# Kernel tuning notes

Measured on AMD Instinct MI355X. Metric: run time of the kernel, lower is better.

The kernel has to match this reference:

```python
import jax, jax.numpy as jnp
import numpy as np

NSLICES = 4
HID = 512
IN_FEAT = 342   # input_shape - 1 (last column is phase)
OUT = 311
BATCH = 256


def cubic(y0, y1, y2, y3, mu):
    # Catmull-Rom cubic interpolation, as in the original PFNN code
    return (
        (-0.5 * y0 + 1.5 * y1 - 1.5 * y2 + 0.5 * y3) * mu * mu * mu
        + (y0 - 2.5 * y1 + 2.0 * y2 - 0.5 * y3) * mu * mu
        + (-0.5 * y0 + 0.5 * y2) * mu
        + y1
    )


def setup_inputs() -> dict:
    key = jax.random.key(0)
    ks = jax.random.split(key, 7)
    x = jax.random.uniform(ks[0], (BATCH, IN_FEAT + 1), dtype=jnp.float32)
    s = 0.02
    W0 = jax.random.normal(ks[1], (NSLICES, HID, IN_FEAT), dtype=jnp.float32) * s
    b0 = jax.random.normal(ks[2], (NSLICES, HID), dtype=jnp.float32) * s
    W1 = jax.random.normal(ks[3], (NSLICES, HID, HID), dtype=jnp.float32) * s
    b1 = jax.random.normal(ks[4], (NSLICES, HID), dtype=jnp.float32) * s
    W2 = jax.random.normal(ks[5], (NSLICES, OUT, HID), dtype=jnp.float32) * s
    b2 = jax.random.normal(ks[6], (NSLICES, OUT), dtype=jnp.float32) * s
    return {"x": x, "W0": W0, "b0": b0, "W1": W1, "b1": b1, "W2": W2, "b2": b2}


def reference(x, W0, b0, W1, b1, W2, b2):
    phase = x[:, -1]                       # [B]
    pscale = NSLICES * phase
    mu = jnp.mod(pscale, 1.0)              # [B]
    i1 = jnp.floor(pscale).astype(jnp.int32) % NSLICES
    i0 = (i1 - 1) % NSLICES
    i2 = (i1 + 1) % NSLICES
    i3 = (i1 + 2) % NSLICES
    muW = mu[:, None, None]                # broadcast over (out, in)
    mub = mu[:, None]

    Wb0 = cubic(W0[i0], W0[i1], W0[i2], W0[i3], muW)   # [B, 512, 342]
    bb0 = cubic(b0[i0], b0[i1], b0[i2], b0[i3], mub)   # [B, 512]
    Wb1 = cubic(W1[i0], W1[i1], W1[i2], W1[i3], muW)   # [B, 512, 512]
    bb1 = cubic(b1[i0], b1[i1], b1[i2], b1[i3], mub)
    Wb2 = cubic(W2[i0], W2[i1], W2[i2], W2[i3], muW)   # [B, 311, 512]
    bb2 = cubic(b2[i0], b2[i1], b2[i2], b2[i3], mub)

    h = x[:, :-1]                                       # [B, 342]
    h = jax.nn.elu(jnp.einsum('boi,bi->bo', Wb0, h) + bb0)
    h = jax.nn.elu(jnp.einsum('boi,bi->bo', Wb1, h) + bb1)
    out = jnp.einsum('boi,bi->bo', Wb2, h) + bb2        # [B, 311]
    return out
```

## Files before the change

kernel.cpp:

```cpp
#include <hip/hip_runtime.h>
#include <math.h>

#define HID 512
#define IN_FEAT 342
#define OUTD 311
#define BATCH 256
#define XROW (IN_FEAT + 1)
#define KP0 352

typedef unsigned short u16;
typedef short bf16x8 __attribute__((ext_vector_type(8)));
typedef float f32x4 __attribute__((ext_vector_type(4)));

__device__ __forceinline__ u16 f2bf_rne(float v) {
    unsigned int x = __float_as_uint(v);
    unsigned int r = (x + 0x7fffu + ((x >> 16) & 1u)) >> 16;
    return (u16)r;
}
__device__ __forceinline__ float bf2f(u16 u) {
    return __uint_as_float(((unsigned int)u) << 16);
}

__device__ __forceinline__ void cvt8(const float* v, bf16x8& hi, bf16x8& lo) {
#pragma unroll
    for (int j = 0; j < 8; j++) {
        unsigned int xu = __float_as_uint(v[j]);
        unsigned int rnd = xu + 0x7fffu + ((xu >> 16) & 1u);
        hi[j] = (short)(rnd >> 16);
        float lof = v[j] - __uint_as_float(rnd & 0xffff0000u);
        lo[j] = (short)(__float_as_uint(lof) >> 16);
    }
}

template<int KCH, int KLDS, int FINAL, int L0>
__global__ __launch_bounds__(256, 2) void layer_direct(
    const float* __restrict__ W,
    int Kw, int Mreal, int Mb,
    const float* __restrict__ x,
    const u16* __restrict__ Hhi, const u16* __restrict__ Hlo,
    const float* __restrict__ bias,
    u16* __restrict__ Ohi, u16* __restrict__ Olo, float* __restrict__ outp)
{
    union SharedU {
        u16 h[2][16 * KLDS];
        float acc[4][16][17];
    };
    __shared__ SharedU sm;

    const int tid = (int)threadIdx.x;
    const int b0 = (int)blockIdx.x * 16;
    const int o0 = (int)blockIdx.y * 16;

    if (L0) {
        for (int idx = tid; idx < 16 * KP0; idx += 256) {
            int r = idx / KP0, k = idx - r * KP0;
            float v = (k < IN_FEAT) ? x[(size_t)(b0 + r) * XROW + k] : 0.f;
            u16 h = f2bf_rne(v);
            sm.h[0][r * KLDS + k] = h;
            sm.h[1][r * KLDS + k] = f2bf_rne(v - bf2f(h));
        }
    } else {
        constexpr int CH = KCH * 4;
        for (int idx = tid; idx < 16 * CH; idx += 256) {
            int r = idx / CH, c = idx - r * CH;
            size_t g = (size_t)(b0 + r) * HID + c * 8;
            *reinterpret_cast<uint4*>(&sm.h[0][r * KLDS + c * 8]) =
                *reinterpret_cast<const uint4*>(Hhi + g);
            *reinterpret_cast<uint4*>(&sm.h[1][r * KLDS + c * 8]) =
                *reinterpret_cast<const uint4*>(Hlo + g);
        }
    }
    __syncthreads();

    const int lane = tid & 63;
    const int s = tid >> 6;
    const int m = lane & 15;
    const int q = lane >> 4;

    int orow = o0 + m;
    if (orow >= Mreal) orow = Mreal - 1;
    const float* wr = W + ((size_t)s * Mreal + orow) * Kw;

    const u16* hp = &sm.h[0][m * KLDS + q * 8];

    f32x4 a0 = {0.f, 0.f, 0.f, 0.f};
    f32x4 a1 = {0.f, 0.f, 0.f, 0.f};
    f32x4 a2 = {0.f, 0.f, 0.f, 0.f};

#pragma unroll
    for (int cc = 0; cc < KCH; ++cc) {
        const int kb = cc * 32 + q * 8;
        float v[8];
        if (L0) {
            if (cc < KCH - 1) {
#pragma unroll
                for (int t = 0; t < 4; t++) {
                    float2 f2 = *reinterpret_cast<const float2*>(wr + kb + t * 2);
                    v[t * 2] = f2.x; v[t * 2 + 1] = f2.y;
                }
            } else {
#pragma unroll
                for (int j = 0; j < 8; j++) {
                    int k = kb + j;
                    v[j] = (k < IN_FEAT) ? wr[k] : 0.f;
                }
            }
        } else {
            float4 f4a = *reinterpret_cast<const float4*>(wr + kb);
            float4 f4b = *reinterpret_cast<const float4*>(wr + kb + 4);
            v[0] = f4a.x; v[1] = f4a.y; v[2] = f4a.z; v[3] = f4a.w;
            v[4] = f4b.x; v[5] = f4b.y; v[6] = f4b.z; v[7] = f4b.w;
        }
        bf16x8 ah, al;
        cvt8(v, ah, al);
        bf16x8 bh = *reinterpret_cast<const bf16x8*>(hp + cc * 32);
        bf16x8 bl = *reinterpret_cast<const bf16x8*>(hp + cc * 32 + 16 * KLDS);
        a0 = __builtin_amdgcn_mfma_f32_16x16x32_bf16(ah, bh, a0, 0, 0, 0);
        a1 = __builtin_amdgcn_mfma_f32_16x16x32_bf16(ah, bl, a1, 0, 0, 0);
        a2 = __builtin_amdgcn_mfma_f32_16x16x32_bf16(al, bh, a2, 0, 0, 0);
    }
    __syncthreads();

    float ds;
    {
        float ps = 4.f * x[(size_t)(b0 + m) * XROW + IN_FEAT];
        float fl = floorf(ps);
        float mu = ps - fl;
        int i1 = ((int)fl) & 3;
        float mu2 = mu * mu, mu3 = mu2 * mu;
        float c0 = -0.5f * mu3 + mu2 - 0.5f * mu;
        float c1 = 1.5f * mu3 - 2.5f * mu2 + 1.0f;
        float c2 = -1.5f * mu3 + 2.0f * mu2 + 0.5f * mu;
        float c3 = 0.5f * mu3 - 0.5f * mu2;
        int k = (s + 1 - i1) & 3;
        ds = (k == 0) ? c0 : (k == 1) ? c1 : (k == 2) ? c2 : c3;
    }

    f32x4 sum = a0 + a1 + a2;
#pragma unroll
    for (int r = 0; r < 4; ++r) {
        int o = o0 + q * 4 + r;
        float bb = (o < Mb) ? bias[(size_t)s * Mb + o] : 0.f;
        sm.acc[s][q * 4 + r][m] = ds * (sum[r] + bb);
    }
    __syncthreads();

    const int o_l = tid & 15;
    const int b_l = tid >> 4;
    float vv = sm.acc[0][o_l][b_l] + sm.acc[1][o_l][b_l]
             + sm.acc[2][o_l][b_l] + sm.acc[3][o_l][b_l];
    const int o = o0 + o_l;
    const int b = b0 + b_l;
    if (!FINAL) {
        float e = (vv > 0.f) ? vv : expm1f(vv);
        u16 h = f2bf_rne(e);
        Ohi[(size_t)b * HID + o] = h;
        Olo[(size_t)b * HID + o] = f2bf_rne(e - bf2f(h));
    } else if (o < OUTD) {
        outp[(size_t)b * OUTD + o] = vv;
    }
}

extern "C" void kernel_launch(void* const* d_in, const int* in_sizes, int n_in,
                              void* d_out, int out_size, void* d_ws, size_t ws_size,
                              hipStream_t stream) {
    const float* x  = (const float*)d_in[0];
    const float* W0 = (const float*)d_in[1];
    const float* b0 = (const float*)d_in[2];
    const float* W1 = (const float*)d_in[3];
    const float* b1 = (const float*)d_in[4];
    const float* W2 = (const float*)d_in[5];
    const float* b2 = (const float*)d_in[6];
    float* out = (float*)d_out;

    char* pw = (char*)d_ws;
    auto alloc = [&](size_t bytes) { char* r = pw; pw += (bytes + 255) & ~(size_t)255; return r; };
    u16* hahi = (u16*)alloc((size_t)BATCH * HID * 2);
    u16* halo = (u16*)alloc((size_t)BATCH * HID * 2);
    u16* hbhi = (u16*)alloc((size_t)BATCH * HID * 2);
    u16* hblo = (u16*)alloc((size_t)BATCH * HID * 2);

    layer_direct<11, 360, 0, 1><<<dim3(BATCH / 16, HID / 16), 256, 0, stream>>>(
        W0, IN_FEAT, HID, HID, x, nullptr, nullptr, b0, hahi, halo, nullptr);

    layer_direct<16, 520, 0, 0><<<dim3(BATCH / 16, HID / 16), 256, 0, stream>>>(
        W1, HID, HID, HID, x, hahi, halo, b1, hbhi, hblo, nullptr);

    layer_direct<16, 520, 1, 0><<<dim3(BATCH / 16, 20), 256, 0, stream>>>(
        W2, HID, OUTD, OUTD, x, hbhi, hblo, b2, nullptr, nullptr, out);
}
```

Measured before the change: 105.5 us.

## Pre-split next layer weights into bf16 hi/lo in previous layer's tail

Each layer kernel now also converts the next layer's fp32 weights into bf16 hi/lo arrays in a grid-stride tail loop, so layers 1 and 2 load bf16 weights directly and skip the per-block conversion. Before this, every batch-tile block re-read the fp32 weights and redid the split, repeating the work 16 times. This adds extra global writes and reads of the converted weights each call, and conversion work is appended to layers 0 and 1.

```diff
diff --git a/kernel.cpp b/kernel.cpp
--- a/kernel.cpp
+++ b/kernel.cpp
@@ -32,14 +32,35 @@
     }
 }
 
-template<int KCH, int KLDS, int FINAL, int L0>
-__global__ __launch_bounds__(256, 2) void layer_direct(
-    const float* __restrict__ W,
-    int Kw, int Mreal, int Mb,
+__device__ __forceinline__ void conv_tail(const float* __restrict__ src,
+                                          u16* __restrict__ dhi, u16* __restrict__ dlo,
+                                          int nchunks)
+{
+    const int bid = (int)blockIdx.y * (int)gridDim.x + (int)blockIdx.x;
+    const int nthr = (int)gridDim.x * (int)gridDim.y * 256;
+    for (int i = bid * 256 + (int)threadIdx.x; i < nchunks; i += nthr) {
+        const float* p = src + (size_t)i * 8;
+        float4 f0 = *reinterpret_cast<const float4*>(p);
+        float4 f1 = *reinterpret_cast<const float4*>(p + 4);
+        float v[8] = {f0.x, f0.y, f0.z, f0.w, f1.x, f1.y, f1.z, f1.w};
+        bf16x8 hi, lo;
+        cvt8(v, hi, lo);
+        *reinterpret_cast<bf16x8*>(dhi + (size_t)i * 8) = hi;
+        *reinterpret_cast<bf16x8*>(dlo + (size_t)i * 8) = lo;
+    }
+}
+
+template<int KCH, int KLDS, int MODE>
+__global__ __launch_bounds__(256, 2) void layer_k(
+    const float* __restrict__ Wf,
+    const u16* __restrict__ Whi, const u16* __restrict__ Wlo,
+    int Wrows,
     const float* __restrict__ x,
     const u16* __restrict__ Hhi, const u16* __restrict__ Hlo,
-    const float* __restrict__ bias,
-    u16* __restrict__ Ohi, u16* __restrict__ Olo, float* __restrict__ outp)
+    const float* __restrict__ bias, int Mb,
+    u16* __restrict__ Ohi, u16* __restrict__ Olo, float* __restrict__ outp,
+    const float* __restrict__ Tsrc, u16* __restrict__ Thi, u16* __restrict__ Tlo,
+    int Tchunks)
 {
     union SharedU {
         u16 h[2][16 * KLDS];
@@ -51,7 +72,7 @@
     const int b0 = (int)blockIdx.x * 16;
     const int o0 = (int)blockIdx.y * 16;
 
-    if (L0) {
+    if (MODE == 0) {
         for (int idx = tid; idx < 16 * KP0; idx += 256) {
             int r = idx / KP0, k = idx - r * KP0;
             float v = (k < IN_FEAT) ? x[(size_t)(b0 + r) * XROW + k] : 0.f;
@@ -78,8 +99,7 @@
     const int q = lane >> 4;
 
     int orow = o0 + m;
-    if (orow >= Mreal) orow = Mreal - 1;
-    const float* wr = W + ((size_t)s * Mreal + orow) * Kw;
+    if (orow >= Wrows) orow = Wrows - 1;
 
     const u16* hp = &sm.h[0][m * KLDS + q * 8];
 
@@ -87,11 +107,12 @@
     f32x4 a1 = {0.f, 0.f, 0.f, 0.f};
     f32x4 a2 = {0.f, 0.f, 0.f, 0.f};
 
-#pragma unroll
-    for (int cc = 0; cc < KCH; ++cc) {
-        const int kb = cc * 32 + q * 8;
-        float v[8];
-        if (L0) {
+    if (MODE == 0) {
+        const float* wr = Wf + ((size_t)s * Wrows + orow) * IN_FEAT;
+#pragma unroll
+        for (int cc = 0; cc < KCH; ++cc) {
+            const int kb = cc * 32 + q * 8;
+            float v[8];
             if (cc < KCH - 1) {
 #pragma unroll
                 for (int t = 0; t < 4; t++) {
@@ -105,19 +126,28 @@
                     v[j] = (k < IN_FEAT) ? wr[k] : 0.f;
                 }
             }
-        } else {
-            float4 f4a = *reinterpret_cast<const float4*>(wr + kb);
-            float4 f4b = *reinterpret_cast<const float4*>(wr + kb + 4);
-            v[0] = f4a.x; v[1] = f4a.y; v[2] = f4a.z; v[3] = f4a.w;
-            v[4] = f4b.x; v[5] = f4b.y; v[6] = f4b.z; v[7] = f4b.w;
-        }
-        bf16x8 ah, al;
-        cvt8(v, ah, al);
-        bf16x8 bh = *reinterpret_cast<const bf16x8*>(hp + cc * 32);
-        bf16x8 bl = *reinterpret_cast<const bf16x8*>(hp + cc * 32 + 16 * KLDS);
-        a0 = __builtin_amdgcn_mfma_f32_16x16x32_bf16(ah, bh, a0, 0, 0, 0);
-        a1 = __builtin_amdgcn_mfma_f32_16x16x32_bf16(ah, bl, a1, 0, 0, 0);
-        a2 = __builtin_amdgcn_mfma_f32_16x16x32_bf16(al, bh, a2, 0, 0, 0);
+            bf16x8 ah, al;
+            cvt8(v, ah, al);
+            bf16x8 bh = *reinterpret_cast<const bf16x8*>(hp + cc * 32);
+            bf16x8 bl = *reinterpret_cast<const bf16x8*>(hp + cc * 32 + 16 * KLDS);
+            a0 = __builtin_amdgcn_mfma_f32_16x16x32_bf16(ah, bh, a0, 0, 0, 0);
+            a1 = __builtin_amdgcn_mfma_f32_16x16x32_bf16(ah, bl, a1, 0, 0, 0);
+            a2 = __builtin_amdgcn_mfma_f32_16x16x32_bf16(al, bh, a2, 0, 0, 0);
+        }
+    } else {
+        const size_t wro = ((size_t)s * Wrows + orow) * (KCH * 32) + q * 8;
+        const u16* wph = Whi + wro;
+        const u16* wpl = Wlo + wro;
+#pragma unroll
+        for (int cc = 0; cc < KCH; ++cc) {
+            bf16x8 ah = *reinterpret_cast<const bf16x8*>(wph + cc * 32);
+            bf16x8 al = *reinterpret_cast<const bf16x8*>(wpl + cc * 32);
+            bf16x8 bh = *reinterpret_cast<const bf16x8*>(hp + cc * 32);
+            bf16x8 bl = *reinterpret_cast<const bf16x8*>(hp + cc * 32 + 16 * KLDS);
+            a0 = __builtin_amdgcn_mfma_f32_16x16x32_bf16(ah, bh, a0, 0, 0, 0);
+            a1 = __builtin_amdgcn_mfma_f32_16x16x32_bf16(ah, bl, a1, 0, 0, 0);
+            a2 = __builtin_amdgcn_mfma_f32_16x16x32_bf16(al, bh, a2, 0, 0, 0);
+        }
     }
     __syncthreads();
 
@@ -151,7 +181,7 @@
              + sm.acc[2][o_l][b_l] + sm.acc[3][o_l][b_l];
     const int o = o0 + o_l;
     const int b = b0 + b_l;
-    if (!FINAL) {
+    if (MODE != 2) {
         float e = (vv > 0.f) ? vv : expm1f(vv);
         u16 h = f2bf_rne(e);
         Ohi[(size_t)b * HID + o] = h;
@@ -159,6 +189,9 @@
     } else if (o < OUTD) {
         outp[(size_t)b * OUTD + o] = vv;
     }
+
+    if (MODE != 2 && Tchunks > 0)
+        conv_tail(Tsrc, Thi, Tlo, Tchunks);
 }
 
 extern "C" void kernel_launch(void* const* d_in, const int* in_sizes, int n_in,
@@ -175,17 +208,27 @@
 
     char* pw = (char*)d_ws;
     auto alloc = [&](size_t bytes) { char* r = pw; pw += (bytes + 255) & ~(size_t)255; return r; };
+    u16* whi1 = (u16*)alloc((size_t)4 * HID * HID * 2);
+    u16* wlo1 = (u16*)alloc((size_t)4 * HID * HID * 2);
+    u16* whi2 = (u16*)alloc((size_t)4 * OUTD * HID * 2);
+    u16* wlo2 = (u16*)alloc((size_t)4 * OUTD * HID * 2);
     u16* hahi = (u16*)alloc((size_t)BATCH * HID * 2);
     u16* halo = (u16*)alloc((size_t)BATCH * HID * 2);
     u16* hbhi = (u16*)alloc((size_t)BATCH * HID * 2);
     u16* hblo = (u16*)alloc((size_t)BATCH * HID * 2);
 
-    layer_direct<11, 360, 0, 1><<<dim3(BATCH / 16, HID / 16), 256, 0, stream>>>(
-        W0, IN_FEAT, HID, HID, x, nullptr, nullptr, b0, hahi, halo, nullptr);
-
-    layer_direct<16, 520, 0, 0><<<dim3(BATCH / 16, HID / 16), 256, 0, stream>>>(
-        W1, HID, HID, HID, x, hahi, halo, b1, hbhi, hblo, nullptr);
-
-    layer_direct<16, 520, 1, 0><<<dim3(BATCH / 16, 20), 256, 0, stream>>>(
-        W2, HID, OUTD, OUTD, x, hbhi, hblo, b2, nullptr, nullptr, out);
-}
+    const int W1_CHUNKS = 4 * HID * HID / 8;
+    const int W2_CHUNKS = 4 * OUTD * HID / 8;
+
+    layer_k<11, 360, 0><<<dim3(BATCH / 16, HID / 16), 256, 0, stream>>>(
+        W0, nullptr, nullptr, HID, x, nullptr, nullptr, b0, HID,
+        hahi, halo, nullptr, W1, whi1, wlo1, W1_CHUNKS);
+
+    layer_k<16, 520, 1><<<dim3(BATCH / 16, HID / 16), 256, 0, stream>>>(
+        nullptr, whi1, wlo1, HID, x, hahi, halo, b1, HID,
+        hbhi, hblo, nullptr, W2, whi2, wlo2, W2_CHUNKS);
+
+    layer_k<16, 520, 2><<<dim3(BATCH / 16, 20), 256, 0, stream>>>(
+        nullptr, whi2, wlo2, OUTD, x, hbhi, hblo, b2, OUTD,
+        nullptr, nullptr, out, nullptr, nullptr, nullptr, 0);
+}
```

After: 106.0 us. No clear change (+0.4%).
